# Kernel optimization log

Measured on AMD Instinct MI355X. Metric: run time of the kernel, lower is better.

The kernel has to match this reference:

```python
import jax, jax.numpy as jnp
import numpy as np

N_NODES = 50000
N_EDGES = 600000
D_IN = 128
D_HID = 128
D_OUT = 40
EPS = 1e-5


def setup_inputs() -> dict:
    key = jax.random.key(0)
    ks = jax.random.split(key, 16)
    inp = {
        "x": jax.random.normal(ks[0], (N_NODES, D_IN), dtype=jnp.float32),
        "edge_index": jax.random.randint(ks[1], (2, N_EDGES), 0, N_NODES, dtype=jnp.int64),
    }
    dims = [(D_IN, D_HID), (D_HID, D_HID), (D_HID, D_OUT)]
    for i, (di, do) in enumerate(dims):
        s = 1.0 / np.sqrt(di)
        inp[f"W_l{i}"] = jax.random.uniform(ks[2 + 3 * i], (di, do), jnp.float32, -s, s)
        inp[f"b_l{i}"] = jax.random.uniform(ks[3 + 3 * i], (do,), jnp.float32, -s, s)
        inp[f"W_r{i}"] = jax.random.uniform(ks[4 + 3 * i], (di, do), jnp.float32, -s, s)
    for i in range(2):  # num_convs - 1 Trans (LayerNorm) blocks
        inp[f"g{i}"] = jnp.ones((D_HID,), jnp.float32)
        inp[f"be{i}"] = jnp.zeros((D_HID,), jnp.float32)
    return inp


def _sage_conv(x, src, dst, W_l, b_l, W_r):
    # mean-aggregate neighbor features at dst, then lin_l(agg) + lin_r(x)
    msg = jax.ops.segment_sum(x[src], dst, num_segments=N_NODES)  # [N, d]
    deg = jax.ops.segment_sum(jnp.ones((src.shape[0],), x.dtype), dst, num_segments=N_NODES)
    agg = msg / jnp.clip(deg, 1.0)[:, None]
    return agg @ W_l + b_l + x @ W_r


def _trans(x, g, b):
    # LayerNorm -> GELU (exact); Dropout p=0 is identity
    mu = jnp.mean(x, axis=-1, keepdims=True)
    var = jnp.mean(jnp.square(x - mu), axis=-1, keepdims=True)
    xn = (x - mu) * jax.lax.rsqrt(var + EPS) * g + b
    return jax.nn.gelu(xn, approximate=False)


def reference(x, edge_index, W_l0, b_l0, W_r0, W_l1, b_l1, W_r1, W_l2, b_l2, W_r2, g0, be0, g1, be1):
    src, dst = edge_index[0], edge_index[1]
    h = _sage_conv(x, src, dst, W_l0, b_l0, W_r0)
    h = _sage_conv(_trans(h, g0, be0), src, dst, W_l1, b_l1, W_r1)
    h = _sage_conv(_trans(h, g1, be1), src, dst, W_l2, b_l2, W_r2)
    return jax.nn.log_softmax(h, axis=1)
```

## Files before the change

### kernel.cpp

```cpp
#include <hip/hip_runtime.h>
#include <math.h>

#define N_NODES 50000
#define N_EDGES 600000
#define DF 128
#define KK 256
#define DOUT 40
#define EPSN 1e-5f
#define NB1 196

typedef __attribute__((ext_vector_type(8))) short sh8;
typedef __attribute__((ext_vector_type(4))) float f32x4;

__device__ __forceinline__ unsigned short f2b(float f) {
  unsigned u = __builtin_bit_cast(unsigned, f);
  unsigned r = u + 0x7FFFu + ((u >> 16) & 1u);
  return (unsigned short)(r >> 16);
}
__device__ __forceinline__ float b2f(unsigned short b) {
  unsigned u = ((unsigned)b) << 16;
  return __builtin_bit_cast(float, u);
}
__device__ __forceinline__ float gelu_f(float x) {
  return 0.5f * x * (1.0f + erff(x * 0.70710678118654752f));
}

__global__ __launch_bounds__(256) void k_prep(
    const int* __restrict__ ei, int* __restrict__ counts,
    const float* __restrict__ x, unsigned* __restrict__ A,
    const float* __restrict__ Wl0, const float* __restrict__ Wr0,
    const float* __restrict__ Wl1, const float* __restrict__ Wr1,
    const float* __restrict__ Wl2, const float* __restrict__ Wr2,
    unsigned short* __restrict__ WT0, unsigned short* __restrict__ WT1,
    unsigned short* __restrict__ WT2b) {
  const int b = blockIdx.x, t = threadIdx.x;
  if (b < 2344) {
    int e = b * 256 + t;
    if (e < N_EDGES) atomicAdd(&counts[ei[N_EDGES + e]], 1);
  } else if (b < 14844) {
    int i = (b - 2344) * 256 + t;
    int n = i >> 6, p = i & 63;
    float2 v = ((const float2*)x)[i];
    A[(size_t)n * 128 + 64 + p] = (unsigned)f2b(v.x) | ((unsigned)f2b(v.y) << 16);
  } else {
    int i = (b - 14844) * 256 + t;
    if (i >= 75776) return;
    if (i < 65536) {
      const float* Wl; const float* Wr; unsigned short* WT; int j;
      if (i < 32768) { j = i;         Wl = Wl0; Wr = Wr0; WT = WT0; }
      else           { j = i - 32768; Wl = Wl1; Wr = Wr1; WT = WT1; }
      int n = j >> 8, k = j & 255;
      float v = (k < DF) ? Wl[k * DF + n] : Wr[(k - DF) * DF + n];
      WT[j] = f2b(v);
    } else {
      int j = i - 65536;
      int n = j >> 7, k = j & 127;
      float v = (n < DOUT) ? Wl2[k * DOUT + n] : Wr2[k * DOUT + (n - DOUT)];
      WT2b[j] = f2b(v);
    }
  }
}

__global__ __launch_bounds__(256) void k_bsum(
    const int* __restrict__ counts, int* __restrict__ bsum) {
  int i = blockIdx.x * 256 + threadIdx.x;
  int v = (i < N_NODES) ? counts[i] : 0;
  #pragma unroll
  for (int m = 1; m < 64; m <<= 1) v += __shfl_xor(v, m);
  __shared__ int ws[4];
  if ((threadIdx.x & 63) == 0) ws[threadIdx.x >> 6] = v;
  __syncthreads();
  if (threadIdx.x == 0) bsum[blockIdx.x] = ws[0] + ws[1] + ws[2] + ws[3];
}

__global__ __launch_bounds__(256) void k_rowptr(
    const int* __restrict__ counts, const int* __restrict__ bsum,
    int* __restrict__ rowptr, int* __restrict__ cursor,
    float* __restrict__ invdeg) {
  const int t = threadIdx.x;
  const int lane = t & 63, w = t >> 6;
  __shared__ int wtot[4], wpre[4];

  int pre = 0;
  for (int i = t; i < blockIdx.x; i += 256) pre += bsum[i];
  #pragma unroll
  for (int m = 1; m < 64; m <<= 1) pre += __shfl_xor(pre, m);
  if (lane == 0) wpre[w] = pre;

  const int i = blockIdx.x * 256 + t;
  int c = (i < N_NODES) ? counts[i] : 0;
  int s = c;
  #pragma unroll
  for (int off = 1; off < 64; off <<= 1) {
    int u = __shfl_up(s, off);
    if (lane >= off) s += u;
  }
  if (lane == 63) wtot[w] = s;
  __syncthreads();
  int add = wpre[0] + wpre[1] + wpre[2] + wpre[3];
  for (int k = 0; k < w; ++k) add += wtot[k];
  if (i < N_NODES) {
    int excl = s - c + add;
    rowptr[i] = excl;
    cursor[i] = excl;
    invdeg[i] = 1.0f / (float)((c > 1) ? c : 1);
  }
  if (blockIdx.x == 0 && t == 0) rowptr[N_NODES] = N_EDGES;
}

__global__ __launch_bounds__(256) void k_fill(
    const int* __restrict__ ei, int* __restrict__ cursor, int* __restrict__ csr) {
  int e = blockIdx.x * 256 + threadIdx.x;
  if (e < N_EDGES) {
    int d = ei[N_EDGES + e];
    int p = atomicAdd(&cursor[d], 1);
    csr[p] = ei[e];
  }
}

__global__ __launch_bounds__(256) void k_agg(
    unsigned* __restrict__ A, const int* __restrict__ rowptr,
    const int* __restrict__ csr, const float* __restrict__ invdeg) {
  const int wid = (blockIdx.x * 256 + threadIdx.x) >> 6;
  const int lane = threadIdx.x & 63;
  const int sg = lane >> 4, l = lane & 15;
  const int node = wid * 4 + sg;
  const int beg = rowptr[node], end = rowptr[node + 1];
  const uint4* H4 = (const uint4*)A;

  float f0=0,f1=0,f2=0,f3=0,f4=0,f5=0,f6=0,f7=0;
  float g0=0,g1=0,g2=0,g3=0,g4=0,g5=0,g6=0,g7=0;
  int j = beg;
  for (; j + 2 <= end; j += 2) {
    int c0 = csr[j], c1 = csr[j + 1];
    uint4 p = H4[(size_t)c0 * 32 + 16 + l];
    uint4 q = H4[(size_t)c1 * 32 + 16 + l];
    f0 += b2f((unsigned short)p.x); f1 += b2f((unsigned short)(p.x >> 16));
    f2 += b2f((unsigned short)p.y); f3 += b2f((unsigned short)(p.y >> 16));
    f4 += b2f((unsigned short)p.z); f5 += b2f((unsigned short)(p.z >> 16));
    f6 += b2f((unsigned short)p.w); f7 += b2f((unsigned short)(p.w >> 16));
    g0 += b2f((unsigned short)q.x); g1 += b2f((unsigned short)(q.x >> 16));
    g2 += b2f((unsigned short)q.y); g3 += b2f((unsigned short)(q.y >> 16));
    g4 += b2f((unsigned short)q.z); g5 += b2f((unsigned short)(q.z >> 16));
    g6 += b2f((unsigned short)q.w); g7 += b2f((unsigned short)(q.w >> 16));
  }
  if (j < end) {
    uint4 p = H4[(size_t)csr[j] * 32 + 16 + l];
    f0 += b2f((unsigned short)p.x); f1 += b2f((unsigned short)(p.x >> 16));
    f2 += b2f((unsigned short)p.y); f3 += b2f((unsigned short)(p.y >> 16));
    f4 += b2f((unsigned short)p.z); f5 += b2f((unsigned short)(p.z >> 16));
    f6 += b2f((unsigned short)p.w); f7 += b2f((unsigned short)(p.w >> 16));
  }
  f0+=g0; f1+=g1; f2+=g2; f3+=g3; f4+=g4; f5+=g5; f6+=g6; f7+=g7;
  const float rd = invdeg[node];
  uint4 o;
  o.x = (unsigned)f2b(f0 * rd) | ((unsigned)f2b(f1 * rd) << 16);
  o.y = (unsigned)f2b(f2 * rd) | ((unsigned)f2b(f3 * rd) << 16);
  o.z = (unsigned)f2b(f4 * rd) | ((unsigned)f2b(f5 * rd) << 16);
  o.w = (unsigned)f2b(f6 * rd) | ((unsigned)f2b(f7 * rd) << 16);
  ((uint4*)A)[(size_t)node * 32 + l] = o;
}

__global__ __launch_bounds__(256) void k_gemm128(
    const unsigned short* __restrict__ Acat, const unsigned short* __restrict__ WT,
    const float* __restrict__ bl, const float* __restrict__ g,
    const float* __restrict__ be, unsigned short* __restrict__ Adst) {
  __shared__ __align__(16) char lds[8704];
  unsigned short* olds = (unsigned short*)lds;
  float2* pp = (float2*)(lds + 8192);

  const int t = threadIdx.x;
  const int rw = blockIdx.x * 16;
  const int wave = t >> 6, lane = t & 63;
  const int lr = lane & 15, lg = lane >> 4;

  #pragma unroll
  for (int it = 0; it < 2; ++it) {
    int id = it * 256 + t;
    int r = id >> 5, c = id & 31;
    sh8 v = *(const sh8*)(Acat + (size_t)(rw + r) * KK + c * 8);
    unsigned off = (unsigned)((r * 512 + c * 16) ^ ((r & 7) << 4));
    *(sh8*)(lds + off) = v;
  }

  sh8 Bfrag[2][8];
  #pragma unroll
  for (int fl = 0; fl < 2; ++fl) {
    const int n = wave * 32 + fl * 16 + lr;
    const sh8* Bp = (const sh8*)(WT + (size_t)n * KK + lg * 8);
    #pragma unroll
    for (int ks = 0; ks < 8; ++ks) Bfrag[fl][ks] = Bp[ks * 4];
  }
  const int col0 = wave * 32 + lr, col1 = col0 + 16;
  const float bc0 = bl[col0], bc1 = bl[col1];
  const float gv0 = g[col0], gv1 = g[col1];
  const float bev0 = be[col0], bev1 = be[col1];

  __syncthreads();

  f32x4 acc0 = {0.f, 0.f, 0.f, 0.f}, acc1 = {0.f, 0.f, 0.f, 0.f};
  #pragma unroll
  for (int ks = 0; ks < 8; ++ks) {
    unsigned off = (unsigned)((lr * 512 + ks * 64 + lg * 16) ^ ((lr & 7) << 4));
    sh8 a = *(const sh8*)(lds + off);
    acc0 = __builtin_amdgcn_mfma_f32_16x16x32_bf16(a, Bfrag[0][ks], acc0, 0, 0, 0);
    acc1 = __builtin_amdgcn_mfma_f32_16x16x32_bf16(a, Bfrag[1][ks], acc1, 0, 0, 0);
  }

  float sv[4], qv[4];
  #pragma unroll
  for (int r = 0; r < 4; ++r) {
    float v0 = acc0[r] + bc0, v1 = acc1[r] + bc1;
    acc0[r] = v0; acc1[r] = v1;
    sv[r] = v0 + v1; qv[r] = v0 * v0 + v1 * v1;
  }
  #pragma unroll
  for (int m = 1; m < 16; m <<= 1) {
    #pragma unroll
    for (int r = 0; r < 4; ++r) {
      sv[r] += __shfl_xor(sv[r], m);
      qv[r] += __shfl_xor(qv[r], m);
    }
  }
  if (lr == 0) {
    #pragma unroll
    for (int r = 0; r < 4; ++r)
      pp[wave * 16 + lg * 4 + r] = make_float2(sv[r], qv[r]);
  }
  __syncthreads();

  #pragma unroll
  for (int r = 0; r < 4; ++r) {
    const int row = lg * 4 + r;
    float2 a0 = pp[row], a1 = pp[16 + row], a2 = pp[32 + row], a3 = pp[48 + row];
    float mu = (a0.x + a1.x + a2.x + a3.x) * (1.0f / 128.0f);
    float var = (a0.y + a1.y + a2.y + a3.y) * (1.0f / 128.0f) - mu * mu;
    float rs = rsqrtf(var + EPSN);
    float xn0 = (acc0[r] - mu) * rs * gv0 + bev0;
    float xn1 = (acc1[r] - mu) * rs * gv1 + bev1;
    olds[row * 136 + col0] = f2b(gelu_f(xn0));
    olds[row * 136 + col1] = f2b(gelu_f(xn1));
  }
  __syncthreads();

  {
    int r = t >> 4, c = t & 15;
    sh8 v = *(const sh8*)((char*)olds + r * 272 + c * 16);
    *(sh8*)(Adst + (size_t)(rw + r) * KK + 128 + c * 8) = v;
  }
}

__global__ __launch_bounds__(256) void k_gemm80(
    const unsigned short* __restrict__ Acat, const unsigned short* __restrict__ WT,
    unsigned short* __restrict__ PQ) {
  __shared__ __align__(16) char lds[16384];
  const int t = threadIdx.x;
  const int rw = blockIdx.x * 64;
  const int wave = t >> 6, lane = t & 63;
  const int lr = lane & 15, lg = lane >> 4;

  #pragma unroll
  for (int it = 0; it < 4; ++it) {
    int id = it * 256 + t;
    int r = id >> 4, c = id & 15;
    int gr = rw + r; if (gr >= N_NODES) gr = N_NODES - 1;
    sh8 v = *(const sh8*)(Acat + (size_t)gr * KK + 128 + c * 8);
    unsigned off = (unsigned)((r * 256 + c * 16) ^ ((r & 7) << 4));
    *(sh8*)(lds + off) = v;
  }

  sh8 Bfrag[5][4];
  #pragma unroll
  for (int f = 0; f < 5; ++f) {
    const int n = f * 16 + lr;
    const sh8* Bp = (const sh8*)(WT + (size_t)n * 128 + lg * 8);
    #pragma unroll
    for (int ks = 0; ks < 4; ++ks) Bfrag[f][ks] = Bp[ks * 4];
  }
  __syncthreads();

  f32x4 accs[5];
  #pragma unroll
  for (int f = 0; f < 5; ++f) accs[f] = (f32x4){0.f, 0.f, 0.f, 0.f};

  #pragma unroll
  for (int ks = 0; ks < 4; ++ks) {
    const int r = wave * 16 + lr;
    unsigned off = (unsigned)((r * 256 + ks * 64 + lg * 16) ^ ((r & 7) << 4));
    sh8 a = *(const sh8*)(lds + off);
    #pragma unroll
    for (int f = 0; f < 5; ++f)
      accs[f] = __builtin_amdgcn_mfma_f32_16x16x32_bf16(a, Bfrag[f][ks], accs[f], 0, 0, 0);
  }
  __syncthreads();

  unsigned short* olds = (unsigned short*)lds;
  #pragma unroll
  for (int f = 0; f < 5; ++f) {
    #pragma unroll
    for (int r = 0; r < 4; ++r) {
      const int row = wave * 16 + lg * 4 + r;
      olds[row * 80 + f * 16 + lr] = f2b(accs[f][r]);
    }
  }
  __syncthreads();

  #pragma unroll
  for (int it = 0; it < 3; ++it) {
    int id = it * 256 + t;
    if (id < 640) {
      int r = (id * 6554) >> 16;
      int c = id - r * 10;
      int gr = rw + r;
      if (gr < N_NODES)
        *(sh8*)(PQ + (size_t)gr * 80 + c * 8) =
            *(const sh8*)((char*)olds + r * 160 + c * 16);
    }
  }
}

__global__ __launch_bounds__(256) void k_final(
    const unsigned short* __restrict__ PQ, const float* __restrict__ bl,
    const int* __restrict__ rowptr, const int* __restrict__ csr,
    const float* __restrict__ invdeg, float* __restrict__ out) {
  const int node = blockIdx.x * 8 + (threadIdx.x >> 5);
  const int hl = threadIdx.x & 31;
  const bool act = (hl < 20);
  const int l = act ? hl : 0;
  const unsigned* Pu = (const unsigned*)PQ;

  const int beg = rowptr[node], end = rowptr[node + 1];
  float ax = 0.f, ay = 0.f, bx = 0.f, by = 0.f;
  float cx = 0.f, cy = 0.f, dx = 0.f, dy = 0.f;
  int j = beg;
  for (; j + 4 <= end; j += 4) {
    int c0 = csr[j], c1 = csr[j + 1], c2 = csr[j + 2], c3 = csr[j + 3];
    unsigned p0 = Pu[(size_t)c0 * 40 + l];
    unsigned p1 = Pu[(size_t)c1 * 40 + l];
    unsigned p2 = Pu[(size_t)c2 * 40 + l];
    unsigned p3 = Pu[(size_t)c3 * 40 + l];
    ax += b2f((unsigned short)p0); ay += b2f((unsigned short)(p0 >> 16));
    bx += b2f((unsigned short)p1); by += b2f((unsigned short)(p1 >> 16));
    cx += b2f((unsigned short)p2); cy += b2f((unsigned short)(p2 >> 16));
    dx += b2f((unsigned short)p3); dy += b2f((unsigned short)(p3 >> 16));
  }
  for (; j < end; ++j) {
    unsigned p = Pu[(size_t)csr[j] * 40 + l];
    ax += b2f((unsigned short)p); ay += b2f((unsigned short)(p >> 16));
  }
  ax += bx + cx + dx;
  ay += by + cy + dy;
  const float rd = invdeg[node];
  unsigned q = Pu[(size_t)node * 40 + 20 + l];
  float v0 = ax * rd + b2f((unsigned short)q) + bl[2 * l];
  float v1 = ay * rd + b2f((unsigned short)(q >> 16)) + bl[2 * l + 1];

  float m = act ? fmaxf(v0, v1) : -INFINITY;
  #pragma unroll
  for (int k = 1; k < 32; k <<= 1) m = fmaxf(m, __shfl_xor(m, k));
  float se = act ? (expf(v0 - m) + expf(v1 - m)) : 0.0f;
  #pragma unroll
  for (int k = 1; k < 32; k <<= 1) se += __shfl_xor(se, k);
  float lse = m + logf(se);
  if (act)
    ((float2*)out)[(size_t)node * 20 + hl] = make_float2(v0 - lse, v1 - lse);
}

extern "C" void kernel_launch(void* const* d_in, const int* in_sizes, int n_in,
                              void* d_out, int out_size, void* d_ws, size_t ws_size,
                              hipStream_t stream) {
  const float* x   = (const float*)d_in[0];
  const int*   ei  = (const int*)d_in[1];
  const float* Wl0 = (const float*)d_in[2];
  const float* bl0 = (const float*)d_in[3];
  const float* Wr0 = (const float*)d_in[4];
  const float* Wl1 = (const float*)d_in[5];
  const float* bl1 = (const float*)d_in[6];
  const float* Wr1 = (const float*)d_in[7];
  const float* Wl2 = (const float*)d_in[8];
  const float* bl2 = (const float*)d_in[9];
  const float* Wr2 = (const float*)d_in[10];
  const float* g0  = (const float*)d_in[11];
  const float* be0 = (const float*)d_in[12];
  const float* g1  = (const float*)d_in[13];
  const float* be1 = (const float*)d_in[14];
  float* out = (float*)d_out;

  unsigned short* A    = (unsigned short*)d_ws;
  unsigned short* PQ   = A + (size_t)N_NODES * KK;
  unsigned short* WT0  = PQ + (size_t)N_NODES * 80;
  unsigned short* WT1  = WT0 + 128 * KK;
  unsigned short* WT2b = WT1 + 128 * KK;
  float* invdeg = (float*)(WT2b + 80 * 128);
  int*   counts = (int*)(invdeg + N_NODES);
  int*   rowptr = counts + N_NODES;
  int*   cursor = rowptr + N_NODES + 1;
  int*   csr    = cursor + N_NODES;
  int*   bsum   = csr + N_EDGES;

  const int egrid = (N_EDGES + 255) / 256;
  const int pgrid = 2344 + 12500 + 296;
  const int agrid = N_NODES / 16;
  const int g128  = N_NODES / 16;
  const int g80   = (N_NODES + 63) / 64;
  const int fgrid = N_NODES / 8;

  hipMemsetAsync(counts, 0, N_NODES * sizeof(int), stream);
  k_prep<<<pgrid, 256, 0, stream>>>(ei, counts, x, (unsigned*)A,
                                    Wl0, Wr0, Wl1, Wr1, Wl2, Wr2,
                                    WT0, WT1, WT2b);
  k_bsum<<<NB1, 256, 0, stream>>>(counts, bsum);
  k_rowptr<<<NB1, 256, 0, stream>>>(counts, bsum, rowptr, cursor, invdeg);
  k_fill<<<egrid, 256, 0, stream>>>(ei, cursor, csr);

  k_agg<<<agrid, 256, 0, stream>>>((unsigned*)A, rowptr, csr, invdeg);
  k_gemm128<<<g128, 256, 0, stream>>>(A, WT0, bl0, g0, be0, A);

  k_agg<<<agrid, 256, 0, stream>>>((unsigned*)A, rowptr, csr, invdeg);
  k_gemm128<<<g128, 256, 0, stream>>>(A, WT1, bl1, g1, be1, A);

  k_gemm80<<<g80, 256, 0, stream>>>(A, WT2b, PQ);
  k_final<<<fgrid, 256, 0, stream>>>(PQ, bl2, rowptr, csr, invdeg, out);
}
```

Baseline: 223.8 us.

## Fuse second SAGE GEMM with final 80-wide projection; drop block-sum kernel

Layer-two GEMM plus LayerNorm/GELU now feeds its bf16 output through LDS straight into the layer-three projection (WT2b), writing only PQ. This removes the global write and reread of the hidden activations and one launch. The separate block-sum kernel is also removed, and each rowptr block now sums all preceding counts directly. That adds redundant prefix reads, up to 50K ints per late block, in exchange for one fewer launch. Wave 0 does extra MFMAs for the fifth output tile, which makes work uneven across waves.

```diff
diff --git a/kernel.cpp b/kernel.cpp
--- a/kernel.cpp
+++ b/kernel.cpp
@@ -61,20 +61,8 @@
   }
 }
 
-__global__ __launch_bounds__(256) void k_bsum(
-    const int* __restrict__ counts, int* __restrict__ bsum) {
-  int i = blockIdx.x * 256 + threadIdx.x;
-  int v = (i < N_NODES) ? counts[i] : 0;
-  #pragma unroll
-  for (int m = 1; m < 64; m <<= 1) v += __shfl_xor(v, m);
-  __shared__ int ws[4];
-  if ((threadIdx.x & 63) == 0) ws[threadIdx.x >> 6] = v;
-  __syncthreads();
-  if (threadIdx.x == 0) bsum[blockIdx.x] = ws[0] + ws[1] + ws[2] + ws[3];
-}
-
 __global__ __launch_bounds__(256) void k_rowptr(
-    const int* __restrict__ counts, const int* __restrict__ bsum,
+    const int* __restrict__ counts,
     int* __restrict__ rowptr, int* __restrict__ cursor,
     float* __restrict__ invdeg) {
   const int t = threadIdx.x;
@@ -82,7 +70,8 @@
   __shared__ int wtot[4], wpre[4];
 
   int pre = 0;
-  for (int i = t; i < blockIdx.x; i += 256) pre += bsum[i];
+  const int limit = blockIdx.x * 256;
+  for (int i = t; i < limit; i += 256) pre += counts[i];
   #pragma unroll
   for (int m = 1; m < 64; m <<= 1) pre += __shfl_xor(pre, m);
   if (lane == 0) wpre[w] = pre;
@@ -250,72 +239,121 @@
   }
 }
 
-__global__ __launch_bounds__(256) void k_gemm80(
+__global__ __launch_bounds__(256) void k_gemm128b(
     const unsigned short* __restrict__ Acat, const unsigned short* __restrict__ WT,
-    unsigned short* __restrict__ PQ) {
-  __shared__ __align__(16) char lds[16384];
+    const float* __restrict__ bl, const float* __restrict__ g,
+    const float* __restrict__ be,
+    const unsigned short* __restrict__ WT2b, unsigned short* __restrict__ PQ) {
+  __shared__ __align__(16) char lds[8704];
+  unsigned short* olds = (unsigned short*)lds;
+  unsigned short* pqs  = (unsigned short*)(lds + 4352);
+  float2* pp = (float2*)(lds + 8192);
+
   const int t = threadIdx.x;
-  const int rw = blockIdx.x * 64;
+  const int rw = blockIdx.x * 16;
   const int wave = t >> 6, lane = t & 63;
   const int lr = lane & 15, lg = lane >> 4;
 
   #pragma unroll
-  for (int it = 0; it < 4; ++it) {
+  for (int it = 0; it < 2; ++it) {
     int id = it * 256 + t;
-    int r = id >> 4, c = id & 15;
-    int gr = rw + r; if (gr >= N_NODES) gr = N_NODES - 1;
-    sh8 v = *(const sh8*)(Acat + (size_t)gr * KK + 128 + c * 8);
-    unsigned off = (unsigned)((r * 256 + c * 16) ^ ((r & 7) << 4));
+    int r = id >> 5, c = id & 31;
+    sh8 v = *(const sh8*)(Acat + (size_t)(rw + r) * KK + c * 8);
+    unsigned off = (unsigned)((r * 512 + c * 16) ^ ((r & 7) << 4));
     *(sh8*)(lds + off) = v;
   }
 
-  sh8 Bfrag[5][4];
-  #pragma unroll
-  for (int f = 0; f < 5; ++f) {
-    const int n = f * 16 + lr;
-    const sh8* Bp = (const sh8*)(WT + (size_t)n * 128 + lg * 8);
-    #pragma unroll
-    for (int ks = 0; ks < 4; ++ks) Bfrag[f][ks] = Bp[ks * 4];
-  }
-  __syncthreads();
-
-  f32x4 accs[5];
-  #pragma unroll
-  for (int f = 0; f < 5; ++f) accs[f] = (f32x4){0.f, 0.f, 0.f, 0.f};
-
+  sh8 Bfrag[2][8];
+  #pragma unroll
+  for (int fl = 0; fl < 2; ++fl) {
+    const int n = wave * 32 + fl * 16 + lr;
+    const sh8* Bp = (const sh8*)(WT + (size_t)n * KK + lg * 8);
+    #pragma unroll
+    for (int ks = 0; ks < 8; ++ks) Bfrag[fl][ks] = Bp[ks * 4];
+  }
+  const int col0 = wave * 32 + lr, col1 = col0 + 16;
+  const float bc0 = bl[col0], bc1 = bl[col1];
+  const float gv0 = g[col0], gv1 = g[col1];
+  const float bev0 = be[col0], bev1 = be[col1];
+
+  __syncthreads();
+
+  f32x4 acc0 = {0.f, 0.f, 0.f, 0.f}, acc1 = {0.f, 0.f, 0.f, 0.f};
+  #pragma unroll
+  for (int ks = 0; ks < 8; ++ks) {
+    unsigned off = (unsigned)((lr * 512 + ks * 64 + lg * 16) ^ ((lr & 7) << 4));
+    sh8 a = *(const sh8*)(lds + off);
+    acc0 = __builtin_amdgcn_mfma_f32_16x16x32_bf16(a, Bfrag[0][ks], acc0, 0, 0, 0);
+    acc1 = __builtin_amdgcn_mfma_f32_16x16x32_bf16(a, Bfrag[1][ks], acc1, 0, 0, 0);
+  }
+
+  sh8 B2[2][4];
+  {
+    const int n = wave * 16 + lr;
+    const sh8* Bp = (const sh8*)(WT2b + (size_t)n * 128 + lg * 8);
+    #pragma unroll
+    for (int ks = 0; ks < 4; ++ks) B2[0][ks] = Bp[ks * 4];
+    const sh8* Bp4 = (const sh8*)(WT2b + (size_t)(64 + lr) * 128 + lg * 8);
+    #pragma unroll
+    for (int ks = 0; ks < 4; ++ks) B2[1][ks] = (wave == 0) ? Bp4[ks * 4] : B2[0][ks];
+  }
+
+  float sv[4], qv[4];
+  #pragma unroll
+  for (int r = 0; r < 4; ++r) {
+    float v0 = acc0[r] + bc0, v1 = acc1[r] + bc1;
+    acc0[r] = v0; acc1[r] = v1;
+    sv[r] = v0 + v1; qv[r] = v0 * v0 + v1 * v1;
+  }
+  #pragma unroll
+  for (int m = 1; m < 16; m <<= 1) {
+    #pragma unroll
+    for (int r = 0; r < 4; ++r) {
+      sv[r] += __shfl_xor(sv[r], m);
+      qv[r] += __shfl_xor(qv[r], m);
+    }
+  }
+  if (lr == 0) {
+    #pragma unroll
+    for (int r = 0; r < 4; ++r)
+      pp[wave * 16 + lg * 4 + r] = make_float2(sv[r], qv[r]);
+  }
+  __syncthreads();
+
+  #pragma unroll
+  for (int r = 0; r < 4; ++r) {
+    const int row = lg * 4 + r;
+    float2 a0 = pp[row], a1 = pp[16 + row], a2 = pp[32 + row], a3 = pp[48 + row];
+    float mu = (a0.x + a1.x + a2.x + a3.x) * (1.0f / 128.0f);
+    float var = (a0.y + a1.y + a2.y + a3.y) * (1.0f / 128.0f) - mu * mu;
+    float rs = rsqrtf(var + EPSN);
+    float xn0 = (acc0[r] - mu) * rs * gv0 + bev0;
+    float xn1 = (acc1[r] - mu) * rs * gv1 + bev1;
+    olds[row * 136 + col0] = f2b(gelu_f(xn0));
+    olds[row * 136 + col1] = f2b(gelu_f(xn1));
+  }
+  __syncthreads();
+
+  f32x4 apq0 = {0.f, 0.f, 0.f, 0.f}, apq1 = {0.f, 0.f, 0.f, 0.f};
   #pragma unroll
   for (int ks = 0; ks < 4; ++ks) {
-    const int r = wave * 16 + lr;
-    unsigned off = (unsigned)((r * 256 + ks * 64 + lg * 16) ^ ((r & 7) << 4));
-    sh8 a = *(const sh8*)(lds + off);
-    #pragma unroll
-    for (int f = 0; f < 5; ++f)
-      accs[f] = __builtin_amdgcn_mfma_f32_16x16x32_bf16(a, Bfrag[f][ks], accs[f], 0, 0, 0);
-  }
-  __syncthreads();
-
-  unsigned short* olds = (unsigned short*)lds;
-  #pragma unroll
-  for (int f = 0; f < 5; ++f) {
-    #pragma unroll
-    for (int r = 0; r < 4; ++r) {
-      const int row = wave * 16 + lg * 4 + r;
-      olds[row * 80 + f * 16 + lr] = f2b(accs[f][r]);
-    }
-  }
-  __syncthreads();
-
-  #pragma unroll
-  for (int it = 0; it < 3; ++it) {
-    int id = it * 256 + t;
-    if (id < 640) {
-      int r = (id * 6554) >> 16;
-      int c = id - r * 10;
-      int gr = rw + r;
-      if (gr < N_NODES)
-        *(sh8*)(PQ + (size_t)gr * 80 + c * 8) =
-            *(const sh8*)((char*)olds + r * 160 + c * 16);
-    }
+    sh8 a = *(const sh8*)((const char*)olds + lr * 272 + ks * 64 + lg * 16);
+    apq0 = __builtin_amdgcn_mfma_f32_16x16x32_bf16(a, B2[0][ks], apq0, 0, 0, 0);
+    apq1 = __builtin_amdgcn_mfma_f32_16x16x32_bf16(a, B2[1][ks], apq1, 0, 0, 0);
+  }
+  #pragma unroll
+  for (int r = 0; r < 4; ++r) {
+    const int row = lg * 4 + r;
+    pqs[row * 80 + wave * 16 + lr] = f2b(apq0[r]);
+    if (wave == 0) pqs[row * 80 + 64 + lr] = f2b(apq1[r]);
+  }
+  __syncthreads();
+
+  if (t < 160) {
+    int r = (t * 6554) >> 16;
+    int c = t - r * 10;
+    *(sh8*)(PQ + (size_t)(rw + r) * 80 + c * 8) =
+        *(const sh8*)((char*)pqs + r * 160 + c * 16);
   }
 }
 
@@ -396,29 +434,25 @@
   int*   rowptr = counts + N_NODES;
   int*   cursor = rowptr + N_NODES + 1;
   int*   csr    = cursor + N_NODES;
-  int*   bsum   = csr + N_EDGES;
 
   const int egrid = (N_EDGES + 255) / 256;
   const int pgrid = 2344 + 12500 + 296;
   const int agrid = N_NODES / 16;
   const int g128  = N_NODES / 16;
-  const int g80   = (N_NODES + 63) / 64;
   const int fgrid = N_NODES / 8;
 
   hipMemsetAsync(counts, 0, N_NODES * sizeof(int), stream);
   k_prep<<<pgrid, 256, 0, stream>>>(ei, counts, x, (unsigned*)A,
                                     Wl0, Wr0, Wl1, Wr1, Wl2, Wr2,
                                     WT0, WT1, WT2b);
-  k_bsum<<<NB1, 256, 0, stream>>>(counts, bsum);
-  k_rowptr<<<NB1, 256, 0, stream>>>(counts, bsum, rowptr, cursor, invdeg);
+  k_rowptr<<<NB1, 256, 0, stream>>>(counts, rowptr, cursor, invdeg);
   k_fill<<<egrid, 256, 0, stream>>>(ei, cursor, csr);
 
   k_agg<<<agrid, 256, 0, stream>>>((unsigned*)A, rowptr, csr, invdeg);
   k_gemm128<<<g128, 256, 0, stream>>>(A, WT0, bl0, g0, be0, A);
 
   k_agg<<<agrid, 256, 0, stream>>>((unsigned*)A, rowptr, csr, invdeg);
-  k_gemm128<<<g128, 256, 0, stream>>>(A, WT1, bl1, g1, be1, A);
-
-  k_gemm80<<<g80, 256, 0, stream>>>(A, WT2b, PQ);
+  k_gemm128b<<<g128, 256, 0, stream>>>(A, WT1, bl1, g1, be1, WT2b, PQ);
+
   k_final<<<fgrid, 256, 0, stream>>>(PQ, bl2, rowptr, csr, invdeg, out);
 }
```

Result: slower. 239.8 us (+7.2%).
